# Performance work log

Measured on AMD Instinct MI355X. Metric: run time of the kernel, lower is better.

The kernel has to match this reference:

```python
import jax, jax.numpy as jnp
import numpy as np
import math

BATCH = 2
SEQ = 2048
D_MODEL = 1024
D_STATE = 16
D_CONV = 4
D_INNER = 2048  # expand_factor * d_model
DT_RANK = 64    # ceil(d_model / 16)
DT_MIN, DT_MAX = 0.001, 0.1


def setup_inputs() -> dict:
    key = jax.random.key(0)
    ks = jax.random.split(key, 6)
    def s(k, shape, fan_in):
        return jax.random.normal(k, shape, jnp.float32) * (fan_in ** -0.5)
    x = jax.random.normal(ks[0], (BATCH, SEQ, D_MODEL), jnp.float32)
    W_in = s(ks[1], (2 * D_INNER, D_MODEL), D_MODEL)          # in_proj.weight
    conv_w = s(ks[2], (D_INNER, 1, D_CONV), D_CONV)            # depthwise conv kernel
    conv_b = jnp.zeros((D_INNER,), jnp.float32)
    W_x = s(ks[3], (DT_RANK + 2 * D_STATE, D_INNER), D_INNER)  # x_proj.weight
    W_dt = s(ks[4], (D_INNER, DT_RANK), DT_RANK)               # dt_proj.weight
    # dt_proj bias init: inverse-softplus of dt ~ LogUniform(dt_min, dt_max)
    rng = np.random.default_rng(0)
    dt = np.exp(rng.uniform(size=D_INNER) * (math.log(DT_MAX) - math.log(DT_MIN)) + math.log(DT_MIN))
    dt = np.clip(dt, DT_MIN, None)
    b_dt = jnp.asarray(dt + np.log(-np.expm1(-dt)), jnp.float32)
    A_log = jnp.log(jnp.broadcast_to(jnp.arange(1, D_STATE + 1, dtype=jnp.float32), (D_INNER, D_STATE)))
    D_param = jnp.ones((D_INNER,), jnp.float32)
    W_out = s(ks[5], (D_MODEL, D_INNER), D_INNER)              # out_proj.weight
    return dict(x=x, W_in=W_in, conv_w=conv_w, conv_b=conv_b, W_x=W_x, W_dt=W_dt,
                b_dt=b_dt, A_log=A_log, D_param=D_param, W_out=W_out)


def _silu(v):
    return v * jax.nn.sigmoid(v)


def _forward(x, W_in, conv_w, conv_b, W_x, W_dt, b_dt, A_log, D_param, W_out):
    # input projection -> (x, z) gates
    xz = x @ W_in.T                       # (B, L, 2*d_inner)
    x_in, z = jnp.split(xz, 2, axis=-1)
    # causal depthwise conv1d (left-pad d_conv-1, matches torch pad+truncate)
    xc = jnp.swapaxes(x_in, 1, 2)         # (B, d_inner, L)
    xc = jax.lax.conv_general_dilated(xc, conv_w, window_strides=(1,),
                                      padding=[(D_CONV - 1, 0)],
                                      feature_group_count=D_INNER)
    xc = xc + conv_b[None, :, None]
    u = _silu(jnp.swapaxes(xc, 1, 2))     # (B, L, d_inner)
    # input-dependent SSM parameters
    x_dbl = u @ W_x.T                     # (B, L, dt_rank + 2*d_state)
    delta_r, Bm, Cm = jnp.split(x_dbl, [DT_RANK, DT_RANK + D_STATE], axis=-1)
    delta = jax.nn.softplus(delta_r @ W_dt.T + b_dt)  # (B, L, d_inner)
    A = -jnp.exp(A_log)                   # (d_inner, d_state)

    def step(state, inp):
        d_t, B_t, C_t, u_t = inp          # (B,d), (B,n), (B,n), (B,d)
        dA = jnp.exp(d_t[..., None] * A)                      # (B, d, n)
        dBu = d_t[..., None] * B_t[:, None, :] * u_t[..., None]
        state = dA * state + dBu          # (B, d, n)
        y = jnp.einsum('bdn,bn->bd', state, C_t)
        return state, y

    xs = (jnp.swapaxes(delta, 0, 1), jnp.swapaxes(Bm, 0, 1),
          jnp.swapaxes(Cm, 0, 1), jnp.swapaxes(u, 0, 1))      # (L, B, ...)
    init = jnp.zeros((x.shape[0], D_INNER, D_STATE), x.dtype)
    _, ys = jax.lax.scan(step, init, xs)  # ys: (L, B, d_inner)
    y = jnp.swapaxes(ys, 0, 1)            # (B, L, d_inner)
    y = y + u * D_param                   # skip connection
    y = y * _silu(z)                      # gating
    return y @ W_out.T                    # (B, L, d_model)


def reference(x, W_in, conv_w, conv_b, W_x, W_dt, b_dt, A_log, D_param, W_out):
    return _forward(x, W_in, conv_w, conv_b, W_x, W_dt, b_dt, A_log, D_param, W_out)
```

## Files before the change

kernel.cpp:

```cpp
#include <hip/hip_runtime.h>
#include <hip/hip_bf16.h>

#define BB 2
#define LL 2048
#define DM 1024
#define DI 2048
#define NSTATE 16
#define DTR 64
#define ROWS (BB*LL)
#define NCH 64
#define LC  32
#define KSPL 8
#define KS4  4

using f32x4  = __attribute__((ext_vector_type(4))) float;
using bf16x8 = __attribute__((ext_vector_type(8))) __bf16;
using s16x8  = __attribute__((ext_vector_type(8))) short;

__device__ __forceinline__ float bf2f(short s){
  unsigned u = ((unsigned)(unsigned short)s) << 16;
  return __builtin_bit_cast(float, u);
}
__device__ __forceinline__ short f2bf(float f){
  unsigned u = __builtin_bit_cast(unsigned, f);
  u += 0x7FFF + ((u >> 16) & 1);
  return (short)(u >> 16);
}

__device__ __forceinline__ void gload_lds16(const void* g, void* l){
  __builtin_amdgcn_global_load_lds(
      (const __attribute__((address_space(1))) unsigned int*)g,
      (__attribute__((address_space(3))) unsigned int*)l,
      16, 0, 0);
}

__global__ __launch_bounds__(256)
void k_cvtall(const float* __restrict__ x, const float* __restrict__ W_in,
              const float* __restrict__ W_dt, const float* __restrict__ W_out,
              const float* __restrict__ W_x,
              short* __restrict__ x_bf, short* __restrict__ Win_bf,
              short* __restrict__ Wdt_bf, short* __restrict__ Wout_bf,
              short* __restrict__ Wx_bf)
{
  int i = blockIdx.x * 256 + threadIdx.x;
  const float* src; short* dst; int off;
  if (i < 1048576){ src = x;    dst = x_bf;    off = i; }
  else if (i < 2097152){ src = W_in;  dst = Win_bf;  off = i - 1048576; }
  else if (i < 2621440){ src = W_out; dst = Wout_bf; off = i - 2097152; }
  else if (i < 2654208){ src = W_dt;  dst = Wdt_bf;  off = i - 2621440; }
  else {
    off = i - 2654208;
    int row = off >> 9;
    short4 o = make_short4(0,0,0,0);
    if (row < 96){
      float4 v = ((const float4*)W_x)[off];
      o = make_short4(f2bf(v.x), f2bf(v.y), f2bf(v.z), f2bf(v.w));
    }
    ((short4*)Wx_bf)[off] = o;
    return;
  }
  float4 v = ((const float4*)src)[off];
  ((short4*)dst)[off] = make_short4(f2bf(v.x), f2bf(v.y), f2bf(v.z), f2bf(v.w));
}

#define STAGE_A(h, kt) do { _Pragma("unroll") for (int i_ = 0; i_ < 2; i_++) \
    gload_lds16(Ag + (size_t)(brow + (h)*128 + i_*64 + srow) * ldab + (kof + (kt)*64 + scol), \
                &lsA[(((kt)&1) ? 16384 : 0) + (h)*8192 + i_*4096 + sldsw]); } while(0)
#define STAGE_B(h, kt) do { _Pragma("unroll") for (int i_ = 0; i_ < 2; i_++) \
    gload_lds16(Bg + (size_t)(bcol + (h)*128 + i_*64 + srow) * ldab + (kof + (kt)*64 + scol), \
                &lsB[(((kt)&1) ? 16384 : 0) + (h)*8192 + i_*4096 + sldsw]); } while(0)

template<int EPI>
__global__ __launch_bounds__(512, 2)
void k_g8(const short* __restrict__ Ag, const short* __restrict__ Bg,
          short* __restrict__ Cb, int ldab, int ldc, int KT, int ncbits,
          int zstart)
{
  __shared__ __align__(16) short lsA[2 * 16384];
  __shared__ __align__(16) short lsB[2 * 16384];
  const int tid = threadIdx.x;
  const int w = tid >> 6, l = tid & 63;
  const int wr = w >> 2, wc = w & 3;
  const int ln = l & 15, kb = l >> 4;
  int id = blockIdx.x;
  id = (id & 7) * 32 + (id >> 3);
  const int nc = id & ((1 << ncbits) - 1);
  const int mr = (id >> ncbits) & 15;
  const int ks = id >> (ncbits + 4);
  const int brow = mr * 256, bcol = nc * 256;
  const int kof  = ks * KT * 64;

  const int srow  = w * 8 + (l >> 3);
  const int scol  = ((l & 7) ^ (l >> 3)) * 8;
  const int sldsw = w * 512;

  f32x4 acc[8][4] = {};
  bf16x8 aF[4][2], bF[2][2];

  STAGE_A(0, 0); STAGE_B(0, 0); STAGE_B(1, 0); STAGE_A(1, 0);
  asm volatile("s_waitcnt vmcnt(4)" ::: "memory");
  __builtin_amdgcn_s_barrier();

  for (int t = 0; t < KT; t++){
    const int cb = (t & 1) * 16384;
    #pragma unroll
    for (int p = 0; p < 4; p++){
      const int mh = p >> 1, nh = p & 1;
      if ((p & 1) == 0){
        #pragma unroll
        for (int mi = 0; mi < 4; mi++)
          #pragma unroll
          for (int ks_ = 0; ks_ < 2; ks_++){
            int row = (mh*4 + mi)*32 + wr*16 + ln;
            int col = (ks_*32 + kb*8) ^ ((ln & 7) << 3);
            aF[mi][ks_] = *(const bf16x8*)&lsA[cb + row*64 + col];
          }
      }
      #pragma unroll
      for (int ni = 0; ni < 2; ni++)
        #pragma unroll
        for (int ks_ = 0; ks_ < 2; ks_++){
          int row = (nh*2 + ni)*64 + wc*16 + ln;
          int col = (ks_*32 + kb*8) ^ ((ln & 7) << 3);
          bF[ni][ks_] = *(const bf16x8*)&lsB[cb + row*64 + col];
        }
      if (t < KT - 1){
        if (p == 0)      STAGE_A(0, t+1);
        else if (p == 1) STAGE_B(0, t+1);
        else if (p == 2) STAGE_B(1, t+1);
        else             STAGE_A(1, t+1);
      }
      __builtin_amdgcn_s_barrier();
      __builtin_amdgcn_s_setprio(1);
      #pragma unroll
      for (int mi = 0; mi < 4; mi++)
        #pragma unroll
        for (int ni = 0; ni < 2; ni++)
          #pragma unroll
          for (int ks_ = 0; ks_ < 2; ks_++)
            acc[mh*4+mi][nh*2+ni] = __builtin_amdgcn_mfma_f32_16x16x32_bf16(
                aF[mi][ks_], bF[ni][ks_], acc[mh*4+mi][nh*2+ni], 0, 0, 0);
      __builtin_amdgcn_s_setprio(0);
      if (p != 2){ asm volatile("s_waitcnt vmcnt(4)" ::: "memory"); }
      __builtin_amdgcn_s_barrier();
    }
  }

  const bool dosilu = (EPI == 0) && (bcol >= zstart);
  #pragma unroll
  for (int m = 0; m < 8; m++)
    #pragma unroll
    for (int n = 0; n < 4; n++)
      #pragma unroll
      for (int r = 0; r < 4; r++){
        int grow = brow + m*32 + wr*16 + kb*4 + r;
        int gcol = bcol + n*64 + wc*16 + ln;
        float v = acc[m][n][r];
        if (EPI == 0){
          if (dosilu) v = v / (1.f + __expf(-v));
          Cb[(size_t)grow * ldc + gcol] = f2bf(v);
        } else {
          Cb[((size_t)ks * 4096 + grow) * ldc + gcol] = f2bf(v);
        }
      }
}

__global__ __launch_bounds__(256)
void k_red4(const short* __restrict__ pb, float* __restrict__ out){
  int i = blockIdx.x * 256 + threadIdx.x;
  const size_t NE = (size_t)4096 * 1024;
  float s[8] = {};
  #pragma unroll
  for (int ks = 0; ks < KS4; ks++){
    s16x8 v = *(const s16x8*)&pb[ks * NE + (size_t)i * 8];
    #pragma unroll
    for (int j = 0; j < 8; j++) s[j] += bf2f(v[j]);
  }
  float4 o0 = make_float4(s[0], s[1], s[2], s[3]);
  float4 o1 = make_float4(s[4], s[5], s[6], s[7]);
  ((float4*)out)[i * 2]     = o0;
  ((float4*)out)[i * 2 + 1] = o1;
}

template<int EPI>
__global__ __launch_bounds__(256)
void k_gemm(const short* __restrict__ A, int lda,
            const short* __restrict__ Bm, int ldb,
            float* __restrict__ Cf, short* __restrict__ Cb, int ldc,
            int K, const float* __restrict__ bias)
{
  __shared__ __align__(16) short lsA[128 * 64];
  __shared__ __align__(16) short lsB[128 * 64];
  const int tid  = threadIdx.x;
  const int wave = tid >> 6, lane = tid & 63;
  const int ln   = lane & 15, kb = lane >> 4;
  const int wr   = wave >> 1, wc = wave & 1;
  const int brow = blockIdx.y * 128, bcol = blockIdx.x * 128;
  const int kof  = blockIdx.z * K;

  f32x4 acc[4][4] = {};

  for (int k0 = 0; k0 < K; k0 += 64){
    #pragma unroll
    for (int i = 0; i < 4; i++){
      int c = i * 4 + wave;
      int e = c * 512 + lane * 8;
      int row = e >> 6, col = e & 63;
      gload_lds16(A + (size_t)(brow + row) * lda + (kof + k0 + col), &lsA[c * 512]);
    }
    #pragma unroll
    for (int i = 0; i < 4; i++){
      int c = i * 4 + wave;
      int e = c * 512 + lane * 8;
      int row = e >> 6, col = e & 63;
      gload_lds16(Bm + (size_t)(bcol + row) * ldb + (kof + k0 + col), &lsB[c * 512]);
    }
    __syncthreads();
    #pragma unroll
    for (int kk = 0; kk < 2; kk++){
      bf16x8 av[4], bv[4];
      #pragma unroll
      for (int m = 0; m < 4; m++)
        av[m] = *(const bf16x8*)&lsA[(wr * 64 + m * 16 + ln) * 64 + kk * 32 + kb * 8];
      #pragma unroll
      for (int n = 0; n < 4; n++)
        bv[n] = *(const bf16x8*)&lsB[(wc * 64 + n * 16 + ln) * 64 + kk * 32 + kb * 8];
      #pragma unroll
      for (int m = 0; m < 4; m++)
        #pragma unroll
        for (int n = 0; n < 4; n++)
          acc[m][n] = __builtin_amdgcn_mfma_f32_16x16x32_bf16(av[m], bv[n], acc[m][n], 0, 0, 0);
    }
    __syncthreads();
  }

  #pragma unroll
  for (int m = 0; m < 4; m++){
    #pragma unroll
    for (int n = 0; n < 4; n++){
      #pragma unroll
      for (int r = 0; r < 4; r++){
        int grow = brow + wr * 64 + m * 16 + kb * 4 + r;
        int gcol = bcol + wc * 64 + n * 16 + ln;
        float v = acc[m][n][r];
        if (EPI == 2){
          v += bias[gcol];
          float sp = (v > 20.f) ? v : logf(1.f + __expf(v));
          Cb[(size_t)grow * ldc + gcol] = f2bf(sp);
        } else {
          Cf[((size_t)blockIdx.z * ROWS + grow) * ldc + gcol] = v;
        }
      }
    }
  }
}

__global__ __launch_bounds__(256)
void k_red2(const float* __restrict__ pbuf, short* __restrict__ xdbl,
            float* __restrict__ Bx, float* __restrict__ Cx)
{
  int i = blockIdx.x * 256 + threadIdx.x;
  int row = i >> 7, col = i & 127;
  float s = 0.f;
  #pragma unroll
  for (int sp = 0; sp < KSPL; sp++)
    s += pbuf[((size_t)sp * ROWS + row) * 128 + col];
  xdbl[i] = f2bf(s);
  if (col >= 64 && col < 96){
    float* dst = (col < 80) ? Bx : Cx;
    dst[(size_t)row * 16 + (col & 15)] = s;
  }
}

__global__ __launch_bounds__(256)
void k_conv(const short* __restrict__ xz, const float* __restrict__ cw,
            const float* __restrict__ cb, short* __restrict__ u)
{
  int d  = blockIdx.x * 256 + threadIdx.x;
  int b  = blockIdx.z;
  int l0 = blockIdx.y * 128;
  float w0 = cw[d * 4 + 0], w1 = cw[d * 4 + 1], w2 = cw[d * 4 + 2], w3 = cw[d * 4 + 3];
  float bias = cb[d];
  size_t base = (size_t)b * LL * 4096 + d;
  float x0 = (l0 >= 3) ? bf2f(xz[base + (size_t)(l0 - 3) * 4096]) : 0.f;
  float x1 = (l0 >= 2) ? bf2f(xz[base + (size_t)(l0 - 2) * 4096]) : 0.f;
  float x2 = (l0 >= 1) ? bf2f(xz[base + (size_t)(l0 - 1) * 4096]) : 0.f;
  for (int l = l0; l < l0 + 128; l++){
    float x3 = bf2f(xz[base + (size_t)l * 4096]);
    float a  = bias + w0 * x0 + w1 * x1 + w2 * x2 + w3 * x3;
    float s  = a / (1.f + __expf(-a));
    u[((size_t)b * LL + l) * 2048 + d] = f2bf(s);
    x0 = x1; x1 = x2; x2 = x3;
  }
}

template<int PASS>
struct Stp { float dt, uu, zz; float4 Bq[4], Cq[4]; };

template<int PASS>
__device__ __forceinline__ void s_load(Stp<PASS>& s, size_t r, int d,
    const short* __restrict__ dlt, const short* __restrict__ u,
    const float* __restrict__ Bx, const float* __restrict__ Cx,
    const short* __restrict__ xz)
{
  s.dt = bf2f(dlt[r * 2048 + d]);
  s.uu = bf2f(u  [r * 2048 + d]);
  const float4* Bp = (const float4*)Bx + r * 4;
  #pragma unroll
  for (int q = 0; q < 4; q++) s.Bq[q] = Bp[q];
  if (PASS == 3){
    const float4* Cp = (const float4*)Cx + r * 4;
    #pragma unroll
    for (int q = 0; q < 4; q++) s.Cq[q] = Cp[q];
    s.zz = bf2f(xz[r * 4096 + 2048 + d]);
  }
}

template<int PASS>
__device__ __forceinline__ void s_step(const Stp<PASS>& s, size_t r, int d,
    float Aln0, float Dv, float* state, float& dtsum, short* __restrict__ y)
{
  float p = exp2f(s.dt * Aln0);
  float pw[16];
  pw[0] = p;
  pw[1] = p * p;
  pw[2] = pw[1] * p;
  pw[3] = pw[1] * pw[1];
  #pragma unroll
  for (int n = 4; n < 8; n++)  pw[n] = pw[3] * pw[n - 4];
  #pragma unroll
  for (int n = 8; n < 16; n++) pw[n] = pw[7] * pw[n - 8];
  float dtu = s.dt * s.uu;
  if (PASS == 1) dtsum += s.dt;
  float yv = 0.f;
  const float* Bf = (const float*)s.Bq;
  const float* Cf = (const float*)s.Cq;
  #pragma unroll
  for (int n = 0; n < 16; n++){
    state[n] = fmaf(pw[n], state[n], dtu * Bf[n]);
    if (PASS == 3) yv = fmaf(state[n], Cf[n], yv);
  }
  if (PASS == 3){
    y[r * 2048 + d] = f2bf((yv + s.uu * Dv) * s.zz);
  }
}

template<int PASS>
__global__ __launch_bounds__(256, 4)
void k_chunk(const short* __restrict__ dlt, const short* __restrict__ u,
             const float* __restrict__ Bx, const float* __restrict__ Cx,
             const short* __restrict__ xz, const float* __restrict__ A_log,
             const float* __restrict__ Dp, float* __restrict__ schunk,
             float* __restrict__ dts, short* __restrict__ y)
{
  const int d = blockIdx.x * 256 + threadIdx.x;
  const int c = blockIdx.y;
  const int b = blockIdx.z;

  const float Aln0 = -__expf(A_log[d * 16]) * 1.44269504088896f;

  float state[16];
  const size_t sbase = ((size_t)(b * NCH + c) * 16) * 2048 + d;
  if (PASS == 1){
    #pragma unroll
    for (int n = 0; n < 16; n++) state[n] = 0.f;
  } else {
    #pragma unroll
    for (int n = 0; n < 16; n++) state[n] = schunk[sbase + (size_t)n * 2048];
  }
  const float Dv = (PASS == 3) ? Dp[d] : 0.f;

  float dtsum = 0.f;
  const size_t r0 = (size_t)b * LL + (size_t)c * LC;

  Stp<PASS> sA, sB;
  s_load<PASS>(sA, r0, d, dlt, u, Bx, Cx, xz);
  for (int j = 0; j < LC; j += 2){
    s_load<PASS>(sB, r0 + j + 1, d, dlt, u, Bx, Cx, xz);
    s_step<PASS>(sA, r0 + j, d, Aln0, Dv, state, dtsum, y);
    int jn = (j + 2 < LC) ? j + 2 : (LC - 1);
    s_load<PASS>(sA, r0 + jn, d, dlt, u, Bx, Cx, xz);
    s_step<PASS>(sB, r0 + j + 1, d, Aln0, Dv, state, dtsum, y);
  }

  if (PASS == 1){
    #pragma unroll
    for (int n = 0; n < 16; n++) schunk[sbase + (size_t)n * 2048] = state[n];
    dts[(size_t)(b * NCH + c) * 2048 + d] = dtsum;
  }
}

__global__ __launch_bounds__(256)
void k_fix(float* __restrict__ schunk, const float* __restrict__ dts,
           const float* __restrict__ A_log)
{
  int i = blockIdx.x * 256 + threadIdx.x;
  int b = i >> 15;
  int nd = i & 32767;
  int n = nd >> 11;
  int d = nd & 2047;
  float Aln = -__expf(A_log[d * 16 + n]) * 1.44269504088896f;
  float s = 0.f;
  #pragma unroll 4
  for (int c = 0; c < NCH; c++){
    size_t idx = ((size_t)(b * NCH + c) << 15) + nd;
    float fin = schunk[idx];
    float ap  = exp2f(Aln * dts[(size_t)(b * NCH + c) * 2048 + d]);
    schunk[idx] = s;
    s = fmaf(ap, s, fin);
  }
}

extern "C" void kernel_launch(void* const* d_in, const int* in_sizes, int n_in,
                              void* d_out, int out_size, void* d_ws, size_t ws_size,
                              hipStream_t stream)
{
  const float* x     = (const float*)d_in[0];
  const float* W_in  = (const float*)d_in[1];
  const float* cw    = (const float*)d_in[2];
  const float* cb    = (const float*)d_in[3];
  const float* W_x   = (const float*)d_in[4];
  const float* W_dt  = (const float*)d_in[5];
  const float* b_dt  = (const float*)d_in[6];
  const float* A_log = (const float*)d_in[7];
  const float* Dp    = (const float*)d_in[8];
  const float* W_out = (const float*)d_in[9];
  float* out = (float*)d_out;

  char* ws = (char*)d_ws;
  short* x_bf    = (short*)ws; ws += (size_t)ROWS * DM * 2;
  short* Win_bf  = (short*)ws; ws += (size_t)(2*DI) * DM * 2;
  short* xz_bf   = (short*)ws; ws += (size_t)ROWS * (2*DI) * 2;
  short* u_bf    = (short*)ws; ws += (size_t)ROWS * DI * 2;
  short* Wx_bf   = (short*)ws; ws += (size_t)128 * DI * 2;
  short* xdbl_bf = (short*)ws; ws += (size_t)ROWS * 128 * 2;
  short* Wdt_bf  = (short*)ws; ws += (size_t)DI * DTR * 2;
  short* dlt_bf  = (short*)ws; ws += (size_t)ROWS * DI * 2;
  short* y_bf    = (short*)ws; ws += (size_t)ROWS * DI * 2;
  short* Wout_bf = (short*)ws; ws += (size_t)DM * DI * 2;
  float* Bf32    = (float*)ws; ws += (size_t)ROWS * 16 * 4;
  float* Cf32    = (float*)ws; ws += (size_t)ROWS * 16 * 4;
  float* schunk  = (float*)ws; ws += (size_t)BB * NCH * 16 * DI * 4;
  float* dts     = (float*)ws; ws += (size_t)BB * NCH * DI * 4;
  float* pbuf    = (float*)ws; ws += (size_t)KSPL * ROWS * 128 * 4;
  if ((size_t)(ws - (char*)d_ws) > ws_size) return;

  short* pbuf4 = (short*)d_ws;

  k_cvtall<<<10624, 256, 0, stream>>>(x, W_in, W_dt, W_out, W_x,
                                      x_bf, Win_bf, Wdt_bf, Wout_bf, Wx_bf);

  k_g8<0><<<256, 512, 0, stream>>>(x_bf, Win_bf, xz_bf, DM, 2*DI, 16, 4, 2048);
  k_conv<<<dim3(8, 16, 2), 256, 0, stream>>>(xz_bf, cw, cb, u_bf);
  k_gemm<4><<<dim3(1, 32, KSPL), 256, 0, stream>>>(u_bf, DI, Wx_bf, DI,
                                                   pbuf, nullptr, 128, DI/KSPL, nullptr);
  k_red2<<<2048, 256, 0, stream>>>(pbuf, xdbl_bf, Bf32, Cf32);
  k_gemm<2><<<dim3(16, 32), 256, 0, stream>>>(xdbl_bf, 128, Wdt_bf, DTR,
                                              nullptr, dlt_bf, DI, DTR, b_dt);
  k_chunk<1><<<dim3(8, NCH, 2), 256, 0, stream>>>(dlt_bf, u_bf, Bf32, Cf32,
                                                  xz_bf, A_log, Dp, schunk, dts, y_bf);
  k_fix<<<256, 256, 0, stream>>>(schunk, dts, A_log);
  k_chunk<3><<<dim3(8, NCH, 2), 256, 0, stream>>>(dlt_bf, u_bf, Bf32, Cf32,
                                                  xz_bf, A_log, Dp, schunk, dts, y_bf);
  k_g8<1><<<256, 512, 0, stream>>>(y_bf, Wout_bf, pbuf4, DI, DM, 8, 2, 1<<30);
  k_red4<<<2048, 256, 0, stream>>>(pbuf4, out);
}
```

Before: 285.6 us.

## Restructure big-GEMM inner loop schedule and store chunk states in bf16

The 256x256 GEMM k-loop moves from four phases, each with its own barrier, to a schedule with fewer barriers. B fragments for both column halves stay in registers, and A fragments are reloaded once per half, so LDS reads and sync points are reduced. The prologue now waits for all loads to finish. Separately, the chunked-scan inter-chunk state buffer is stored as bf16 instead of fp32, halving its memory traffic at the cost of lower precision in the carried scan states.

```diff
diff --git a/kernel.cpp b/kernel.cpp
--- a/kernel.cpp
+++ b/kernel.cpp
@@ -95,53 +95,97 @@
   const int sldsw = w * 512;
 
   f32x4 acc[8][4] = {};
-  bf16x8 aF[4][2], bF[2][2];
+  bf16x8 aF[4][2];
+  bf16x8 bF[2][2][2];
 
   STAGE_A(0, 0); STAGE_B(0, 0); STAGE_B(1, 0); STAGE_A(1, 0);
-  asm volatile("s_waitcnt vmcnt(4)" ::: "memory");
+  asm volatile("s_waitcnt vmcnt(0)" ::: "memory");
   __builtin_amdgcn_s_barrier();
 
   for (int t = 0; t < KT; t++){
     const int cb = (t & 1) * 16384;
     #pragma unroll
-    for (int p = 0; p < 4; p++){
-      const int mh = p >> 1, nh = p & 1;
-      if ((p & 1) == 0){
-        #pragma unroll
-        for (int mi = 0; mi < 4; mi++)
-          #pragma unroll
-          for (int ks_ = 0; ks_ < 2; ks_++){
-            int row = (mh*4 + mi)*32 + wr*16 + ln;
-            int col = (ks_*32 + kb*8) ^ ((ln & 7) << 3);
-            aF[mi][ks_] = *(const bf16x8*)&lsA[cb + row*64 + col];
-          }
+    for (int mi = 0; mi < 4; mi++)
+      #pragma unroll
+      for (int ksl = 0; ksl < 2; ksl++){
+        int row = mi*32 + wr*16 + ln;
+        int col = (ksl*32 + kb*8) ^ ((ln & 7) << 3);
+        aF[mi][ksl] = *(const bf16x8*)&lsA[cb + row*64 + col];
       }
+    #pragma unroll
+    for (int ni = 0; ni < 2; ni++)
+      #pragma unroll
+      for (int ksl = 0; ksl < 2; ksl++){
+        int row = ni*64 + wc*16 + ln;
+        int col = (ksl*32 + kb*8) ^ ((ln & 7) << 3);
+        bF[0][ni][ksl] = *(const bf16x8*)&lsB[cb + row*64 + col];
+      }
+    if (t < KT - 1){ STAGE_A(0, t+1); STAGE_B(0, t+1); }
+    __builtin_amdgcn_s_setprio(1);
+    #pragma unroll
+    for (int mi = 0; mi < 4; mi++)
       #pragma unroll
       for (int ni = 0; ni < 2; ni++)
         #pragma unroll
-        for (int ks_ = 0; ks_ < 2; ks_++){
-          int row = (nh*2 + ni)*64 + wc*16 + ln;
-          int col = (ks_*32 + kb*8) ^ ((ln & 7) << 3);
-          bF[ni][ks_] = *(const bf16x8*)&lsB[cb + row*64 + col];
-        }
-      if (t < KT - 1){
-        if (p == 0)      STAGE_A(0, t+1);
-        else if (p == 1) STAGE_B(0, t+1);
-        else if (p == 2) STAGE_B(1, t+1);
-        else             STAGE_A(1, t+1);
+        for (int ksl = 0; ksl < 2; ksl++)
+          acc[mi][ni] = __builtin_amdgcn_mfma_f32_16x16x32_bf16(
+              aF[mi][ksl], bF[0][ni][ksl], acc[mi][ni], 0, 0, 0);
+    __builtin_amdgcn_s_setprio(0);
+    if (t < KT - 1) asm volatile("s_waitcnt vmcnt(4)" ::: "memory");
+    else            asm volatile("s_waitcnt vmcnt(0)" ::: "memory");
+    __builtin_amdgcn_s_barrier();
+
+    #pragma unroll
+    for (int ni = 0; ni < 2; ni++)
+      #pragma unroll
+      for (int ksl = 0; ksl < 2; ksl++){
+        int row = (2 + ni)*64 + wc*16 + ln;
+        int col = (ksl*32 + kb*8) ^ ((ln & 7) << 3);
+        bF[1][ni][ksl] = *(const bf16x8*)&lsB[cb + row*64 + col];
       }
-      __builtin_amdgcn_s_barrier();
-      __builtin_amdgcn_s_setprio(1);
-      #pragma unroll
-      for (int mi = 0; mi < 4; mi++)
+    if (t < KT - 1){ STAGE_B(1, t+1); STAGE_A(1, t+1); }
+    __builtin_amdgcn_s_setprio(1);
+    #pragma unroll
+    for (int mi = 0; mi < 4; mi++)
+      #pragma unroll
+      for (int ni = 0; ni < 2; ni++)
         #pragma unroll
-        for (int ni = 0; ni < 2; ni++)
-          #pragma unroll
-          for (int ks_ = 0; ks_ < 2; ks_++)
-            acc[mh*4+mi][nh*2+ni] = __builtin_amdgcn_mfma_f32_16x16x32_bf16(
-                aF[mi][ks_], bF[ni][ks_], acc[mh*4+mi][nh*2+ni], 0, 0, 0);
-      __builtin_amdgcn_s_setprio(0);
-      if (p != 2){ asm volatile("s_waitcnt vmcnt(4)" ::: "memory"); }
+        for (int ksl = 0; ksl < 2; ksl++)
+          acc[mi][2+ni] = __builtin_amdgcn_mfma_f32_16x16x32_bf16(
+              aF[mi][ksl], bF[1][ni][ksl], acc[mi][2+ni], 0, 0, 0);
+    __builtin_amdgcn_s_setprio(0);
+
+    #pragma unroll
+    for (int mi = 0; mi < 4; mi++)
+      #pragma unroll
+      for (int ksl = 0; ksl < 2; ksl++){
+        int row = (4 + mi)*32 + wr*16 + ln;
+        int col = (ksl*32 + kb*8) ^ ((ln & 7) << 3);
+        aF[mi][ksl] = *(const bf16x8*)&lsA[cb + row*64 + col];
+      }
+    __builtin_amdgcn_s_setprio(1);
+    #pragma unroll
+    for (int mi = 0; mi < 4; mi++)
+      #pragma unroll
+      for (int ni = 0; ni < 2; ni++)
+        #pragma unroll
+        for (int ksl = 0; ksl < 2; ksl++)
+          acc[4+mi][ni] = __builtin_amdgcn_mfma_f32_16x16x32_bf16(
+              aF[mi][ksl], bF[0][ni][ksl], acc[4+mi][ni], 0, 0, 0);
+    __builtin_amdgcn_s_setprio(0);
+
+    __builtin_amdgcn_s_setprio(1);
+    #pragma unroll
+    for (int mi = 0; mi < 4; mi++)
+      #pragma unroll
+      for (int ni = 0; ni < 2; ni++)
+        #pragma unroll
+        for (int ksl = 0; ksl < 2; ksl++)
+          acc[4+mi][2+ni] = __builtin_amdgcn_mfma_f32_16x16x32_bf16(
+              aF[mi][ksl], bF[1][ni][ksl], acc[4+mi][2+ni], 0, 0, 0);
+    __builtin_amdgcn_s_setprio(0);
+    if (t < KT - 1){
+      asm volatile("s_waitcnt vmcnt(4)" ::: "memory");
       __builtin_amdgcn_s_barrier();
     }
   }
@@ -350,7 +394,7 @@
 void k_chunk(const short* __restrict__ dlt, const short* __restrict__ u,
              const float* __restrict__ Bx, const float* __restrict__ Cx,
              const short* __restrict__ xz, const float* __restrict__ A_log,
-             const float* __restrict__ Dp, float* __restrict__ schunk,
+             const float* __restrict__ Dp, short* __restrict__ schunk,
              float* __restrict__ dts, short* __restrict__ y)
 {
   const int d = blockIdx.x * 256 + threadIdx.x;
@@ -366,7 +410,7 @@
     for (int n = 0; n < 16; n++) state[n] = 0.f;
   } else {
     #pragma unroll
-    for (int n = 0; n < 16; n++) state[n] = schunk[sbase + (size_t)n * 2048];
+    for (int n = 0; n < 16; n++) state[n] = bf2f(schunk[sbase + (size_t)n * 2048]);
   }
   const float Dv = (PASS == 3) ? Dp[d] : 0.f;
 
@@ -385,13 +429,13 @@
 
   if (PASS == 1){
     #pragma unroll
-    for (int n = 0; n < 16; n++) schunk[sbase + (size_t)n * 2048] = state[n];
+    for (int n = 0; n < 16; n++) schunk[sbase + (size_t)n * 2048] = f2bf(state[n]);
     dts[(size_t)(b * NCH + c) * 2048 + d] = dtsum;
   }
 }
 
 __global__ __launch_bounds__(256)
-void k_fix(float* __restrict__ schunk, const float* __restrict__ dts,
+void k_fix(short* __restrict__ schunk, const float* __restrict__ dts,
            const float* __restrict__ A_log)
 {
   int i = blockIdx.x * 256 + threadIdx.x;
@@ -404,9 +448,9 @@
   #pragma unroll 4
   for (int c = 0; c < NCH; c++){
     size_t idx = ((size_t)(b * NCH + c) << 15) + nd;
-    float fin = schunk[idx];
+    float fin = bf2f(schunk[idx]);
     float ap  = exp2f(Aln * dts[(size_t)(b * NCH + c) * 2048 + d]);
-    schunk[idx] = s;
+    schunk[idx] = f2bf(s);
     s = fmaf(ap, s, fin);
   }
 }
@@ -440,7 +484,7 @@
   short* Wout_bf = (short*)ws; ws += (size_t)DM * DI * 2;
   float* Bf32    = (float*)ws; ws += (size_t)ROWS * 16 * 4;
   float* Cf32    = (float*)ws; ws += (size_t)ROWS * 16 * 4;
-  float* schunk  = (float*)ws; ws += (size_t)BB * NCH * 16 * DI * 4;
+  short* schunk  = (short*)ws; ws += (size_t)BB * NCH * 16 * DI * 2;
   float* dts     = (float*)ws; ws += (size_t)BB * NCH * DI * 4;
   float* pbuf    = (float*)ws; ws += (size_t)KSPL * ROWS * 128 * 4;
   if ((size_t)(ws - (char*)d_ws) > ws_size) return;
```

Result: faster. 279.4 us (-2.2%).
